# Performance work log

Hardware: AMD Instinct MI355X
Metric: run time of the kernel (lower is better)

## Reference

```python
import jax, jax.numpy as jnp
import numpy as np

N = 50000      # nodes
E = 400000     # edges
IN = 128       # in_channels
HID = 64       # hidden_channels (per head)
H = 4          # heads
OUT = 10       # classes
G = 64         # graphs in batch


def setup_inputs() -> dict:
    key = jax.random.key(0)
    ks = jax.random.split(key, 32)
    s = 0.05
    inp = {
        "x": jax.random.normal(ks[0], (N, IN), dtype=jnp.float32),
        "edge_index": jax.random.randint(ks[1], (2, E), 0, N, dtype=jnp.int32),
        "batch": jnp.sort(jax.random.randint(ks[2], (N,), 0, G, dtype=jnp.int32)),
    }
    # TransformerConv layer 1 params (in=IN -> heads*HID)
    d1 = H * HID
    inp["Wq1"] = jax.random.normal(ks[3], (IN, d1)) * s
    inp["bq1"] = jnp.zeros((d1,), jnp.float32)
    inp["Wk1"] = jax.random.normal(ks[4], (IN, d1)) * s
    inp["bk1"] = jnp.zeros((d1,), jnp.float32)
    inp["Wv1"] = jax.random.normal(ks[5], (IN, d1)) * s
    inp["bv1"] = jnp.zeros((d1,), jnp.float32)
    inp["Ws1"] = jax.random.normal(ks[6], (IN, d1)) * s   # root/skip weight
    inp["bs1"] = jnp.zeros((d1,), jnp.float32)
    # TransformerConv layer 2 params (in=H*HID -> heads*HID)
    inp["Wq2"] = jax.random.normal(ks[7], (d1, d1)) * s
    inp["bq2"] = jnp.zeros((d1,), jnp.float32)
    inp["Wk2"] = jax.random.normal(ks[8], (d1, d1)) * s
    inp["bk2"] = jnp.zeros((d1,), jnp.float32)
    inp["Wv2"] = jax.random.normal(ks[9], (d1, d1)) * s
    inp["bv2"] = jnp.zeros((d1,), jnp.float32)
    inp["Ws2"] = jax.random.normal(ks[10], (d1, d1)) * s
    inp["bs2"] = jnp.zeros((d1,), jnp.float32)
    # final classifier
    inp["Wl"] = jax.random.normal(ks[11], (d1, OUT)) * s
    inp["bl"] = jnp.zeros((OUT,), jnp.float32)
    return inp


def transformer_conv(x, src, dst, Wq, bq, Wk, bk, Wv, bv, Ws, bs):
    """PyG TransformerConv (concat=True, root_weight=True, beta=None, eval mode).
    src = edge_index[0] (source j), dst = edge_index[1] (target i).
    """
    n = x.shape[0]
    q = (x @ Wq + bq).reshape(n, H, HID)
    k = (x @ Wk + bk).reshape(n, H, HID)
    v = (x @ Wv + bv).reshape(n, H, HID)
    # per-edge attention logits [E, H]
    alpha = jnp.einsum('ehc,ehc->eh', q[dst], k[src]) / np.sqrt(HID).astype(np.float32)
    # scatter-softmax over incoming edges of each target node
    amax = jax.ops.segment_max(alpha, dst, num_segments=n)           # [N, H], -inf for isolated
    ex = jnp.exp(alpha - amax[dst])                                   # [E, H]
    denom = jax.ops.segment_sum(ex, dst, num_segments=n) + 1e-16      # [N, H]
    w = ex / denom[dst]                                               # normalized alpha [E, H]
    # scatter-sum aggregation of weighted values
    out = jax.ops.segment_sum(w[:, :, None] * v[src], dst, num_segments=n)  # [N, H, HID]
    out = out.reshape(n, H * HID)
    return out + (x @ Ws + bs)  # root/skip connection


def reference(x, edge_index, batch,
              Wq1, bq1, Wk1, bk1, Wv1, bv1, Ws1, bs1,
              Wq2, bq2, Wk2, bk2, Wv2, bv2, Ws2, bs2,
              Wl, bl):
    src, dst = edge_index[0], edge_index[1]
    h = jax.nn.elu(transformer_conv(x, src, dst, Wq1, bq1, Wk1, bk1, Wv1, bv1, Ws1, bs1))
    h = jax.nn.elu(transformer_conv(h, src, dst, Wq2, bq2, Wk2, bk2, Wv2, bv2, Ws2, bs2))
    # global mean pool per graph
    sums = jax.ops.segment_sum(h, batch, num_segments=G)              # [G, H*HID]
    cnt = jax.ops.segment_sum(jnp.ones((h.shape[0],), h.dtype), batch, num_segments=G)
    pooled = sums / jnp.maximum(cnt, 1.0)[:, None]
    logits = pooled @ Wl + bl
    return jax.nn.log_softmax(logits, axis=-1)
```

## Files before the change

kernel.cpp:

```cpp
#include <hip/hip_runtime.h>
#include <math.h>

constexpr int NN   = 50000;
constexpr int NE   = 400000;
constexpr int INC  = 128;
constexpr int NH   = 4;
constexpr int D1   = 256;
constexpr int D4   = 1024;
constexpr int NOUT = 10;
constexpr int NG   = 64;
constexpr int NB_SCAN = (NN + 255) / 256;


typedef __attribute__((ext_vector_type(8))) short bf16x8;
typedef __attribute__((ext_vector_type(4))) float f32x4;
typedef __attribute__((ext_vector_type(2))) float f32x2;

__device__ __forceinline__ short f2b(float f) {
  union { float f; unsigned int i; } v; v.f = f;
  unsigned int x = v.i;
  return (short)((x + 0x7FFFu + ((x >> 16) & 1u)) >> 16);
}
__device__ __forceinline__ float b2f(short u) {
  union { unsigned int i; float f; } v; v.i = ((unsigned int)(unsigned short)u) << 16;
  return v.f;
}
__device__ __forceinline__ float4 ld4b(const short* p) {
  short4 u = *(const short4*)p;
  return make_float4(b2f(u.x), b2f(u.y), b2f(u.z), b2f(u.w));
}
__device__ __forceinline__ int cvt_pk_bf16(float lo, float hi) {
  int r;
  asm volatile("v_cvt_pk_bf16_f32 %0, %1, %2" : "=v"(r) : "v"(lo), "v"(hi));
  return r;
}
__device__ __forceinline__ int pk_fp8x4(float a, float b, float c, float d) {
  int v = __builtin_amdgcn_cvt_pk_fp8_f32(a, b, 0, false);
  v = __builtin_amdgcn_cvt_pk_fp8_f32(c, d, v, true);
  return v;
}

__device__ __forceinline__ void gld_lds16(const short* g, short* l) {
  __builtin_amdgcn_global_load_lds(
      (const __attribute__((address_space(1))) unsigned int*)g,
      (__attribute__((address_space(3))) unsigned int*)l, 16, 0, 0);
}

constexpr int CVT_XB  = (NN * INC / 4 + 255) / 256;
constexpr int CVT_W1B = (4 * D1 * INC + 255) / 256;
constexpr int CVT_W2B = (4 * D1 * D1 + 255) / 256;
constexpr int CVT_BB  = 8;
constexpr int CVT_DB  = (NN + 255) / 256;
constexpr int CVT_SB  = (NG * D1 + 255) / 256;

__device__ __forceinline__ void wt_one(const float* Wq, const float* Wk,
    const float* Wv, const float* Ws, short* Wt, int kbits, int i) {
  int K = 1 << kbits;
  int seg = i >> (kbits + 8);
  int rem = i & ((D1 << kbits) - 1);
  int n = rem & (D1 - 1), k = rem >> 8;
  const float* W = (seg == 0) ? Wq : (seg == 1) ? Wk : (seg == 2) ? Wv : Ws;
  int row;
  if (seg == 0)      row = n;
  else if (seg == 3) row = 768 + n;
  else               row = 256 + (n >> 2) * 8 + ((seg == 2) ? 4 : 0) + (n & 3);
  Wt[(size_t)row * K + k] = f2b(W[(size_t)k * D1 + n]);
}

__global__ void cvt_all_k(const float* __restrict__ x, short* __restrict__ Xb,
    const float* __restrict__ Wq1, const float* __restrict__ Wk1,
    const float* __restrict__ Wv1, const float* __restrict__ Ws1,
    const float* __restrict__ Wq2, const float* __restrict__ Wk2,
    const float* __restrict__ Wv2, const float* __restrict__ Ws2,
    short* __restrict__ Wtc1, short* __restrict__ Wtc2,
    const float* __restrict__ bq1, const float* __restrict__ bk1,
    const float* __restrict__ bv1, const float* __restrict__ bs1,
    const float* __restrict__ bq2, const float* __restrict__ bk2,
    const float* __restrict__ bv2, const float* __restrict__ bs2,
    float* __restrict__ bc1, float* __restrict__ bc2,
    int* __restrict__ deg, float* __restrict__ sums) {
  const int b = blockIdx.x;
  const int t = threadIdx.x;
  if (b < CVT_XB) {
    int i = (b * 256 + t) * 4;
    if (i >= NN * INC) return;
    float4 v = *(const float4*)(x + i);
    short4 o; o.x = f2b(v.x); o.y = f2b(v.y); o.z = f2b(v.z); o.w = f2b(v.w);
    *(short4*)(Xb + i) = o;
  } else if (b < CVT_XB + CVT_W1B) {
    int i = (b - CVT_XB) * 256 + t;
    if (i < 4 * D1 * INC) wt_one(Wq1, Wk1, Wv1, Ws1, Wtc1, 7, i);
  } else if (b < CVT_XB + CVT_W1B + CVT_W2B) {
    int i = (b - CVT_XB - CVT_W1B) * 256 + t;
    if (i < 4 * D1 * D1) wt_one(Wq2, Wk2, Wv2, Ws2, Wtc2, 8, i);
  } else if (b < CVT_XB + CVT_W1B + CVT_W2B + CVT_BB) {
    int i = (b - CVT_XB - CVT_W1B - CVT_W2B) * 256 + t;
    if (i >= 2 * D4) return;
    int row = i & (D4 - 1);
    const float* bq = (i < D4) ? bq1 : bq2;
    const float* bk = (i < D4) ? bk1 : bk2;
    const float* bv = (i < D4) ? bv1 : bv2;
    const float* bs = (i < D4) ? bs1 : bs2;
    float v;
    if (row < 256) v = bq[row];
    else if (row < 768) {
      int j = row - 256, grp = j >> 3, off = j & 7;
      int ch = grp * 4 + (off & 3);
      v = (off < 4) ? bk[ch] : bv[ch];
    } else v = bs[row - 768];
    ((i < D4) ? bc1 : bc2)[row] = v;
  } else if (b < CVT_XB + CVT_W1B + CVT_W2B + CVT_BB + CVT_DB) {
    int i = (b - CVT_XB - CVT_W1B - CVT_W2B - CVT_BB) * 256 + t;
    if (i < NN) deg[i] = 0;
  } else {
    int i = (b - CVT_XB - CVT_W1B - CVT_W2B - CVT_BB - CVT_DB) * 256 + t;
    if (i < NG * D1) sums[i] = 0.f;
  }
}

__global__ void deg_count(const int* __restrict__ dst, int* __restrict__ deg) {
  int e = blockIdx.x * 256 + threadIdx.x;
  if (e < NE) atomicAdd(&deg[dst[e]], 1);
}
__global__ __launch_bounds__(256) void scan1(const int* __restrict__ deg,
    int* __restrict__ partial, const int* __restrict__ batch, int* __restrict__ gb) {
  if (blockIdx.x == NB_SCAN) {
    int g = threadIdx.x;
    if (g > NG) return;
    int lo = 0, hi = NN;
    while (lo < hi) {
      int mid = (lo + hi) >> 1;
      if (batch[mid] < g) lo = mid + 1; else hi = mid;
    }
    gb[g] = lo;
    return;
  }
  __shared__ int sh[256];
  int t = threadIdx.x, i = blockIdx.x * 256 + t;
  sh[t] = (i < NN) ? deg[i] : 0;
  __syncthreads();
  for (int off = 128; off > 0; off >>= 1) {
    if (t < off) sh[t] += sh[t + off];
    __syncthreads();
  }
  if (t == 0) partial[blockIdx.x] = sh[0];
}
__global__ __launch_bounds__(256) void scan3(const int* __restrict__ deg,
    const int* __restrict__ partial, int* __restrict__ rowstart,
    int* __restrict__ cursor) {
  __shared__ int sh[256];
  __shared__ int base_s;
  const int t = threadIdx.x;
  int pv = (t < NB_SCAN) ? partial[t] : 0;
  sh[t] = pv;
  __syncthreads();
  for (int off = 1; off < 256; off <<= 1) {
    int o = (t >= off) ? sh[t - off] : 0;
    __syncthreads();
    sh[t] += o;
    __syncthreads();
  }
  if (t == 0) base_s = (blockIdx.x == 0) ? 0 : sh[blockIdx.x - 1];
  __syncthreads();
  const int base = base_s;
  __syncthreads();
  int i = blockIdx.x * 256 + t;
  int v = (i < NN) ? deg[i] : 0;
  sh[t] = v;
  __syncthreads();
  for (int off = 1; off < 256; off <<= 1) {
    int o = (t >= off) ? sh[t - off] : 0;
    __syncthreads();
    sh[t] += o;
    __syncthreads();
  }
  int excl = sh[t] - v + base;
  if (i <= NN) rowstart[i] = excl;
  if (i < NN)  cursor[i]   = excl;
}
__global__ void scatter_k(const int* __restrict__ src, const int* __restrict__ dst,
    int* __restrict__ cursor, int* __restrict__ esrc) {
  int e = blockIdx.x * 256 + threadIdx.x;
  if (e >= NE) return;
  int d = dst[e];
  int pos = atomicAdd(&cursor[d], 1);
  esrc[pos] = src[e];
}

constexpr int CLDS = 136;

__global__ __launch_bounds__(256, 4) void gemm_mfma(
    const short* __restrict__ Xb, const short* __restrict__ Wt,
    const float* __restrict__ bias, short* __restrict__ QS,
    unsigned char* __restrict__ KV8, int M, int K) {
  __shared__ short smem[16384];
  const int bx = blockIdx.x;
  const int by = blockIdx.y;
  const int m_tile = (bx & 7) + (by << 3);
  const int n_tile = bx >> 3;
  const int m0 = m_tile * 128;
  if (m0 >= M) return;
  const int n0 = n_tile * 128;

  const int t    = threadIdx.x;
  const int lane = t & 63;
  const int wv   = t >> 6;
  const int wm   = (wv >> 1) * 64;
  const int wn   = (wv & 1) * 64;
  const int quad = lane >> 4;
  const int l16  = lane & 15;
  const int lrow = lane >> 2;
  const int lseg = lane & 3;

  const int swz_w = (lseg ^ ((lrow >> 1) & 3)) * 8;
  const int swz_r = (quad ^ ((l16 >> 1) & 3)) * 8;

  f32x4 acc[4][4] = {};

  {
#pragma unroll
    for (int j = 0; j < 2; ++j) {
      const int rb = (wv * 2 + j) * 16;
      int gm = m0 + rb + lrow;
      gm = gm < M ? gm : M - 1;
      gld_lds16(Xb + (size_t)gm * K + swz_w,              &smem[rb * 32]);
      gld_lds16(Wt + (size_t)(n0 + rb + lrow) * K + swz_w, &smem[4096 + rb * 32]);
    }
  }
  __syncthreads();

  int cur = 0;
  for (int k0 = 0; k0 < K; k0 += 32) {
    if (k0 + 32 < K) {
      short* An = &smem[(cur ^ 1) * 8192];
      short* Bn = &smem[(cur ^ 1) * 8192 + 4096];
#pragma unroll
      for (int j = 0; j < 2; ++j) {
        const int rb = (wv * 2 + j) * 16;
        int gm = m0 + rb + lrow;
        gm = gm < M ? gm : M - 1;
        gld_lds16(Xb + (size_t)gm * K + k0 + 32 + swz_w,              &An[rb * 32]);
        gld_lds16(Wt + (size_t)(n0 + rb + lrow) * K + k0 + 32 + swz_w, &Bn[rb * 32]);
      }
    }
    {
      const short* Ac = &smem[cur * 8192];
      const short* Bc = &smem[cur * 8192 + 4096];
      bf16x8 a[4], b[4];
#pragma unroll
      for (int mi = 0; mi < 4; mi++)
        a[mi] = *(const bf16x8*)(&Ac[(wm + mi * 16 + l16) * 32 + swz_r]);
#pragma unroll
      for (int nj = 0; nj < 4; nj++)
        b[nj] = *(const bf16x8*)(&Bc[(wn + nj * 16 + l16) * 32 + swz_r]);
#pragma unroll
      for (int mi = 0; mi < 4; mi++)
#pragma unroll
        for (int nj = 0; nj < 4; nj++)
          acc[mi][nj] = __builtin_amdgcn_mfma_f32_16x16x32_bf16(b[nj], a[mi], acc[mi][nj], 0, 0, 0);
    }
    __syncthreads();
    cur ^= 1;
  }

  const bool isKV = (n_tile >= 2) && (n_tile <= 5);
  float4 bz[4];
#pragma unroll
  for (int nj = 0; nj < 4; nj++)
    bz[nj] = *(const float4*)(bias + n0 + wn + nj * 16 + quad * 4);
  const int kv_base = n0 - 256;
  const int qs_base = (n_tile < 2) ? n0 : (n0 - 512);

#pragma unroll
  for (int p = 0; p < 2; ++p) {
    if ((wv >> 1) == p) {
      if (isKV) {
        unsigned char* cs = (unsigned char*)smem;
#pragma unroll
        for (int mi = 0; mi < 4; mi++) {
          const int row = mi * 16 + l16;
#pragma unroll
          for (int nj = 0; nj < 4; nj++) {
            const int colb = wn + nj * 16 + quad * 4;
            const int pk = pk_fp8x4(acc[mi][nj][0] + bz[nj].x, acc[mi][nj][1] + bz[nj].y,
                                    acc[mi][nj][2] + bz[nj].z, acc[mi][nj][3] + bz[nj].w);
            *(int*)(cs + row * 136 + colb) = pk;
          }
        }
      } else {
#pragma unroll
        for (int mi = 0; mi < 4; mi++) {
          const int row = mi * 16 + l16;
#pragma unroll
          for (int nj = 0; nj < 4; nj++) {
            const int col = wn + nj * 16 + quad * 4;
            int2 o;
            o.x = cvt_pk_bf16(acc[mi][nj][0] + bz[nj].x, acc[mi][nj][1] + bz[nj].y);
            o.y = cvt_pk_bf16(acc[mi][nj][2] + bz[nj].z, acc[mi][nj][3] + bz[nj].w);
            *(int2*)(&smem[row * CLDS + col]) = o;
          }
        }
      }
    }
    __syncthreads();
    if (isKV) {
      const unsigned char* cs = (const unsigned char*)smem;
#pragma unroll
      for (int it = 0; it < 4; ++it) {
        const int chunk = it * 256 + t;
        const int row = chunk >> 4;
        const int cb  = (chunk & 15) * 8;
        const int gm  = m0 + p * 64 + row;
        if (gm < M)
          *(int2*)(KV8 + (size_t)gm * 512 + kv_base + cb) = *(const int2*)(cs + row * 136 + cb);
      }
    } else {
#pragma unroll
      for (int it = 0; it < 4; ++it) {
        const int chunk = it * 256 + t;
        const int row = chunk >> 4;
        const int cc  = (chunk & 15) * 8;
        const int gm  = m0 + p * 64 + row;
        if (gm < M)
          *(int4*)(QS + (size_t)gm * 512 + qs_base + cc) = *(const int4*)(&smem[row * CLDS + cc]);
      }
    }
    if (p == 0) __syncthreads();
  }
}

__device__ __forceinline__ f32x2 cvt_lo(int x) { return __builtin_amdgcn_cvt_pk_f32_fp8(x, false); }
__device__ __forceinline__ f32x2 cvt_hi(int x) { return __builtin_amdgcn_cvt_pk_f32_fp8(x, true); }

template <int CTRL>
__device__ __forceinline__ float ror_add(float x) {
  int y = __builtin_amdgcn_update_dpp(0, __float_as_int(x), CTRL, 0xF, 0xF, true);
  return x + __int_as_float(y);
}
__device__ __forceinline__ float red16(float x) {
  x = ror_add<0x121>(x);
  x = ror_add<0x122>(x);
  x = ror_add<0x124>(x);
  x = ror_add<0x128>(x);
  return x;
}

#define SC2 (0.125f * 1.44269504088896341f)

__device__ __forceinline__ float edge_score(const int2 x, f32x2 q01, f32x2 q23,
                                            f32x2& vv01, f32x2& vv23) {
  f32x2 kk01 = cvt_lo(x.x), kk23 = cvt_hi(x.x);
  vv01 = cvt_lo(x.y); vv23 = cvt_hi(x.y);
  f32x2 dd = q01 * kk01;
  dd += q23 * kk23;
  return red16(dd.x + dd.y);
}

template <typename TOUT>
__device__ __forceinline__ void st1(TOUT* p, float v);
template <> __device__ __forceinline__ void st1<float>(float* p, float v) { *p = v; }
template <> __device__ __forceinline__ void st1<short>(short* p, float v) { *p = f2b(v); }

template <typename TOUT>
__global__ __launch_bounds__(256) void node_attn(
    const int* __restrict__ rowstart, const int* __restrict__ esrc,
    const short* __restrict__ QS, const unsigned char* __restrict__ KV8,
    TOUT* __restrict__ out) {
  const int nid = blockIdx.x * 4 + (threadIdx.x >> 6);
  if (nid >= NN) return;
  const int t  = threadIdx.x & 63;
  const int c0 = t * 4;
  const int r0 = __builtin_amdgcn_readfirstlane(rowstart[nid]);
  const int r1 = __builtin_amdgcn_readfirstlane(rowstart[nid + 1]);
  const short4 qu = *(const short4*)(QS + (size_t)nid * 512 + c0);
  const f32x2 q01 = {b2f(qu.x) * SC2, b2f(qu.y) * SC2};
  const f32x2 q23 = {b2f(qu.z) * SC2, b2f(qu.w) * SC2};
  const unsigned char* kvb = KV8 + t * 8;
  float m = -INFINITY, denom = 0.f;
  f32x2 a01 = {0.f, 0.f}, a23 = {0.f, 0.f};
  int r = r0;
  for (; r + 7 < r1; r += 8) {
    const int e0 = __builtin_amdgcn_readfirstlane(esrc[r + 0]);
    const int e1 = __builtin_amdgcn_readfirstlane(esrc[r + 1]);
    const int e2 = __builtin_amdgcn_readfirstlane(esrc[r + 2]);
    const int e3 = __builtin_amdgcn_readfirstlane(esrc[r + 3]);
    const int e4 = __builtin_amdgcn_readfirstlane(esrc[r + 4]);
    const int e5 = __builtin_amdgcn_readfirstlane(esrc[r + 5]);
    const int e6 = __builtin_amdgcn_readfirstlane(esrc[r + 6]);
    const int e7 = __builtin_amdgcn_readfirstlane(esrc[r + 7]);
    const int2 x0 = *(const int2*)(kvb + (size_t)e0 * 512);
    const int2 x1 = *(const int2*)(kvb + (size_t)e1 * 512);
    const int2 x2 = *(const int2*)(kvb + (size_t)e2 * 512);
    const int2 x3 = *(const int2*)(kvb + (size_t)e3 * 512);
    const int2 x4 = *(const int2*)(kvb + (size_t)e4 * 512);
    const int2 x5 = *(const int2*)(kvb + (size_t)e5 * 512);
    const int2 x6 = *(const int2*)(kvb + (size_t)e6 * 512);
    const int2 x7 = *(const int2*)(kvb + (size_t)e7 * 512);
    f32x2 v01_0, v23_0, v01_1, v23_1, v01_2, v23_2, v01_3, v23_3;
    f32x2 v01_4, v23_4, v01_5, v23_5, v01_6, v23_6, v01_7, v23_7;
    const float s0 = edge_score(x0, q01, q23, v01_0, v23_0);
    const float s1 = edge_score(x1, q01, q23, v01_1, v23_1);
    const float s2 = edge_score(x2, q01, q23, v01_2, v23_2);
    const float s3 = edge_score(x3, q01, q23, v01_3, v23_3);
    const float s4 = edge_score(x4, q01, q23, v01_4, v23_4);
    const float s5 = edge_score(x5, q01, q23, v01_5, v23_5);
    const float s6 = edge_score(x6, q01, q23, v01_6, v23_6);
    const float s7 = edge_score(x7, q01, q23, v01_7, v23_7);
    const float t01 = fmaxf(s0, s1), t23 = fmaxf(s2, s3);
    const float t45 = fmaxf(s4, s5), t67 = fmaxf(s6, s7);
    const float nm = fmaxf(fmaxf(m, fmaxf(t01, t23)), fmaxf(t45, t67));
    const float sc  = exp2f(m - nm);
    const float ex0 = exp2f(s0 - nm);
    const float ex1 = exp2f(s1 - nm);
    const float ex2 = exp2f(s2 - nm);
    const float ex3 = exp2f(s3 - nm);
    const float ex4 = exp2f(s4 - nm);
    const float ex5 = exp2f(s5 - nm);
    const float ex6 = exp2f(s6 - nm);
    const float ex7 = exp2f(s7 - nm);
    denom = denom * sc + ((ex0 + ex1) + (ex2 + ex3)) + ((ex4 + ex5) + (ex6 + ex7));
    const f32x2 scv = {sc, sc};
    a01 = a01 * scv; a23 = a23 * scv;
    a01 += f32x2{ex0, ex0} * v01_0; a23 += f32x2{ex0, ex0} * v23_0;
    a01 += f32x2{ex1, ex1} * v01_1; a23 += f32x2{ex1, ex1} * v23_1;
    a01 += f32x2{ex2, ex2} * v01_2; a23 += f32x2{ex2, ex2} * v23_2;
    a01 += f32x2{ex3, ex3} * v01_3; a23 += f32x2{ex3, ex3} * v23_3;
    a01 += f32x2{ex4, ex4} * v01_4; a23 += f32x2{ex4, ex4} * v23_4;
    a01 += f32x2{ex5, ex5} * v01_5; a23 += f32x2{ex5, ex5} * v23_5;
    a01 += f32x2{ex6, ex6} * v01_6; a23 += f32x2{ex6, ex6} * v23_6;
    a01 += f32x2{ex7, ex7} * v01_7; a23 += f32x2{ex7, ex7} * v23_7;
    m = nm;
  }
  for (; r + 3 < r1; r += 4) {
    const int e0 = __builtin_amdgcn_readfirstlane(esrc[r + 0]);
    const int e1 = __builtin_amdgcn_readfirstlane(esrc[r + 1]);
    const int e2 = __builtin_amdgcn_readfirstlane(esrc[r + 2]);
    const int e3 = __builtin_amdgcn_readfirstlane(esrc[r + 3]);
    const int2 x0 = *(const int2*)(kvb + (size_t)e0 * 512);
    const int2 x1 = *(const int2*)(kvb + (size_t)e1 * 512);
    const int2 x2 = *(const int2*)(kvb + (size_t)e2 * 512);
    const int2 x3 = *(const int2*)(kvb + (size_t)e3 * 512);
    f32x2 v01_0, v23_0, v01_1, v23_1, v01_2, v23_2, v01_3, v23_3;
    const float s0 = edge_score(x0, q01, q23, v01_0, v23_0);
    const float s1 = edge_score(x1, q01, q23, v01_1, v23_1);
    const float s2 = edge_score(x2, q01, q23, v01_2, v23_2);
    const float s3 = edge_score(x3, q01, q23, v01_3, v23_3);
    const float nm = fmaxf(fmaxf(m, fmaxf(s0, s1)), fmaxf(s2, s3));
    const float sc  = exp2f(m - nm);
    const float ex0 = exp2f(s0 - nm);
    const float ex1 = exp2f(s1 - nm);
    const float ex2 = exp2f(s2 - nm);
    const float ex3 = exp2f(s3 - nm);
    denom = denom * sc + ex0 + ex1 + ex2 + ex3;
    const f32x2 scv = {sc, sc};
    a01 = a01 * scv; a23 = a23 * scv;
    a01 += f32x2{ex0, ex0} * v01_0; a23 += f32x2{ex0, ex0} * v23_0;
    a01 += f32x2{ex1, ex1} * v01_1; a23 += f32x2{ex1, ex1} * v23_1;
    a01 += f32x2{ex2, ex2} * v01_2; a23 += f32x2{ex2, ex2} * v23_2;
    a01 += f32x2{ex3, ex3} * v01_3; a23 += f32x2{ex3, ex3} * v23_3;
    m = nm;
  }
  for (; r < r1; r++) {
    const int e0 = __builtin_amdgcn_readfirstlane(esrc[r]);
    const int2 x0 = *(const int2*)(kvb + (size_t)e0 * 512);
    f32x2 v01_0, v23_0;
    const float s0 = edge_score(x0, q01, q23, v01_0, v23_0);
    const float nm = fmaxf(m, s0);
    const float sc  = exp2f(m - nm);
    const float ex0 = exp2f(s0 - nm);
    denom = denom * sc + ex0;
    const f32x2 scv = {sc, sc};
    a01 = a01 * scv; a23 = a23 * scv;
    a01 += f32x2{ex0, ex0} * v01_0; a23 += f32x2{ex0, ex0} * v23_0;
    m = nm;
  }
  const float inv = 1.0f / (denom + 1e-16f);
  const float4 sk = ld4b(QS + (size_t)nid * 512 + 256 + c0);
  float o0 = a01.x * inv + sk.x;
  float o1 = a01.y * inv + sk.y;
  float o2 = a23.x * inv + sk.z;
  float o3 = a23.y * inv + sk.w;
  o0 = o0 > 0.f ? o0 : expm1f(o0);
  o1 = o1 > 0.f ? o1 : expm1f(o1);
  o2 = o2 > 0.f ? o2 : expm1f(o2);
  o3 = o3 > 0.f ? o3 : expm1f(o3);
  TOUT* p = out + (size_t)nid * D1 + c0;
  st1<TOUT>(p + 0, o0); st1<TOUT>(p + 1, o1);
  st1<TOUT>(p + 2, o2); st1<TOUT>(p + 3, o3);
}

__global__ __launch_bounds__(256) void pool_k(const short* __restrict__ h,
    const int* __restrict__ batch, const int* __restrict__ gb,
    float* __restrict__ sums) {
  const int c = threadIdx.x;
  const int n0 = blockIdx.x * 64;
  const int n1 = min(n0 + 64, NN);
  const int g0 = batch[n0];
  const int g1 = batch[n1 - 1];
  for (int g = g0; g <= g1; ++g) {
    const int a = max(gb[g], n0);
    const int b = min(gb[g + 1], n1);
    if (b <= a) continue;
    float s0 = 0.f, s1 = 0.f, s2 = 0.f, s3 = 0.f;
    int n = a;
    for (; n + 3 < b; n += 4) {
      s0 += b2f(h[(size_t)(n + 0) * D1 + c]);
      s1 += b2f(h[(size_t)(n + 1) * D1 + c]);
      s2 += b2f(h[(size_t)(n + 2) * D1 + c]);
      s3 += b2f(h[(size_t)(n + 3) * D1 + c]);
    }
    for (; n < b; ++n) s0 += b2f(h[(size_t)n * D1 + c]);
    atomicAdd(&sums[(size_t)g * D1 + c], (s0 + s1) + (s2 + s3));
  }
}

__global__ __launch_bounds__(640) void head_k(const float* __restrict__ sums,
    const int* __restrict__ gb, const float* __restrict__ Wl,
    const float* __restrict__ bl, float* __restrict__ out) {
  __shared__ float logits[NG][NOUT];
  const int t = threadIdx.x;
  if (t < NG * NOUT) {
    int g = t / NOUT, o = t % NOUT;
    float inv = 1.0f / fmaxf((float)(gb[g + 1] - gb[g]), 1.0f);
    float acc = 0.f;
    for (int k = 0; k < D1; k++) acc += sums[(size_t)g * D1 + k] * Wl[k * NOUT + o];
    logits[g][o] = acc * inv + bl[o];
  }
  __syncthreads();
  if (t < NG) {
    float mx = -INFINITY;
#pragma unroll
    for (int o = 0; o < NOUT; o++) mx = fmaxf(mx, logits[t][o]);
    float s = 0.f;
#pragma unroll
    for (int o = 0; o < NOUT; o++) s += __expf(logits[t][o] - mx);
    float lse = mx + logf(s);
#pragma unroll
    for (int o = 0; o < NOUT; o++) out[t * NOUT + o] = logits[t][o] - lse;
  }
}

extern "C" void kernel_launch(void* const* d_in, const int* in_sizes, int n_in,
                              void* d_out, int out_size, void* d_ws, size_t ws_size,
                              hipStream_t stream) {
  const float* x   = (const float*)d_in[0];
  const int* ei    = (const int*)d_in[1];
  const int* batch = (const int*)d_in[2];
  const float* Wq1 = (const float*)d_in[3];  const float* bq1 = (const float*)d_in[4];
  const float* Wk1 = (const float*)d_in[5];  const float* bk1 = (const float*)d_in[6];
  const float* Wv1 = (const float*)d_in[7];  const float* bv1 = (const float*)d_in[8];
  const float* Ws1 = (const float*)d_in[9];  const float* bs1 = (const float*)d_in[10];
  const float* Wq2 = (const float*)d_in[11]; const float* bq2 = (const float*)d_in[12];
  const float* Wk2 = (const float*)d_in[13]; const float* bk2 = (const float*)d_in[14];
  const float* Wv2 = (const float*)d_in[15]; const float* bv2 = (const float*)d_in[16];
  const float* Ws2 = (const float*)d_in[17]; const float* bs2 = (const float*)d_in[18];
  const float* Wl  = (const float*)d_in[19]; const float* bl  = (const float*)d_in[20];

  const int* srcIdx = ei;
  const int* dstIdx = ei + NE;

  float* ws = (float*)d_ws;
  const size_t SZ_NODE = (size_t)NN * D1;
  float* H2f  = ws;
  short* H2b  = (short*)H2f;
  float* sums = ws + SZ_NODE;
  float* bc1  = sums + (size_t)NG * D1;
  float* bc2  = bc1 + D4;
  short* Xb   = (short*)(bc2 + D4);
  short* H1b  = Xb + (size_t)NN * INC;
  short* QS   = H1b + SZ_NODE;
  short* Wtc1 = QS + (size_t)NN * 512;
  short* Wtc2 = Wtc1 + (size_t)D4 * INC;
  unsigned char* KV8 = (unsigned char*)(Wtc2 + (size_t)D4 * D1);
  int* ip      = (int*)(KV8 + (size_t)NN * 512);
  int* deg     = ip;
  int* partial = deg + NN;
  int* rowstart= partial + 256;
  int* cursor  = rowstart + NN + 1;
  int* esrc    = cursor + NN;
  int* gb      = esrc + NE;

  const int mtiles = (NN + 127) / 128;
  const dim3 gemmGrid(64, (mtiles + 7) / 8);
  const int edgeBlocks = (NE + 255) / 256;
  const int aggBlocks  = (NN + 3) / 4;
  const int cvtBlocks  = CVT_XB + CVT_W1B + CVT_W2B + CVT_BB + CVT_DB + CVT_SB;

  cvt_all_k<<<cvtBlocks, 256, 0, stream>>>(x, Xb,
      Wq1, Wk1, Wv1, Ws1, Wq2, Wk2, Wv2, Ws2, Wtc1, Wtc2,
      bq1, bk1, bv1, bs1, bq2, bk2, bv2, bs2, bc1, bc2, deg, sums);

  deg_count<<<edgeBlocks, 256, 0, stream>>>(dstIdx, deg);
  scan1<<<NB_SCAN + 1, 256, 0, stream>>>(deg, partial, batch, gb);
  scan3<<<NB_SCAN, 256, 0, stream>>>(deg, partial, rowstart, cursor);
  scatter_k<<<edgeBlocks, 256, 0, stream>>>(srcIdx, dstIdx, cursor, esrc);

  gemm_mfma<<<gemmGrid, 256, 0, stream>>>(Xb, Wtc1, bc1, QS, KV8, NN, INC);
  node_attn<short><<<aggBlocks, 256, 0, stream>>>(rowstart, esrc, QS, KV8, H1b);

  gemm_mfma<<<gemmGrid, 256, 0, stream>>>(H1b, Wtc2, bc2, QS, KV8, NN, D1);
  node_attn<short><<<aggBlocks, 256, 0, stream>>>(rowstart, esrc, QS, KV8, H2b);

  pool_k<<<(NN + 63) / 64, 256, 0, stream>>>(H2b, batch, gb, sums);
  head_k<<<1, 640, 0, stream>>>(sums, gb, Wl, bl, (float*)d_out);
}
```

Measured before the change: 341.5 us.

## Fuse scan into single-pass decoupled lookback, merge pool and head, vectorize weight conversion

Replaces the two-kernel degree scan with one kernel that uses a decoupled-lookback prefix scan with atomic descriptors. It also fuses global mean pooling and the classifier head into a single kernel with one block per graph, which removes the sums buffer and its atomics. Weight transposition now writes 8 bf16 values per thread as one 16-byte store. Together these cut launch count and atomic traffic. In exchange, the lookback spin depends on forward progress across blocks, and the pool kernel has only 64 blocks for the full node reduction.

```diff
diff --git a/kernel.cpp b/kernel.cpp
--- a/kernel.cpp
+++ b/kernel.cpp
@@ -47,24 +47,31 @@
 }
 
 constexpr int CVT_XB  = (NN * INC / 4 + 255) / 256;
-constexpr int CVT_W1B = (4 * D1 * INC + 255) / 256;
-constexpr int CVT_W2B = (4 * D1 * D1 + 255) / 256;
+constexpr int CVT_W1B = (4 * D1 * INC / 8 + 255) / 256;
+constexpr int CVT_W2B = (4 * D1 * D1 / 8 + 255) / 256;
 constexpr int CVT_BB  = 8;
 constexpr int CVT_DB  = (NN + 255) / 256;
-constexpr int CVT_SB  = (NG * D1 + 255) / 256;
-
-__device__ __forceinline__ void wt_one(const float* Wq, const float* Wk,
+constexpr int CVT_FB  = 1;
+
+__device__ __forceinline__ void wt_one8(const float* Wq, const float* Wk,
     const float* Wv, const float* Ws, short* Wt, int kbits, int i) {
-  int K = 1 << kbits;
-  int seg = i >> (kbits + 8);
-  int rem = i & ((D1 << kbits) - 1);
-  int n = rem & (D1 - 1), k = rem >> 8;
+  const int K = 1 << kbits;
+  const int row = i >> (kbits - 3);
+  const int k0 = (i & ((K >> 3) - 1)) << 3;
+  int seg, n;
+  if (row < 256)      { seg = 0; n = row; }
+  else if (row < 768) { int j = row - 256, off = j & 7;
+                        seg = (off >= 4) ? 2 : 1; n = (j >> 3) * 4 + (off & 3); }
+  else                { seg = 3; n = row - 768; }
   const float* W = (seg == 0) ? Wq : (seg == 1) ? Wk : (seg == 2) ? Wv : Ws;
-  int row;
-  if (seg == 0)      row = n;
-  else if (seg == 3) row = 768 + n;
-  else               row = 256 + (n >> 2) * 8 + ((seg == 2) ? 4 : 0) + (n & 3);
-  Wt[(size_t)row * K + k] = f2b(W[(size_t)k * D1 + n]);
+  short o[8];
+#pragma unroll
+  for (int kk = 0; kk < 8; kk++) o[kk] = f2b(W[(size_t)(k0 + kk) * D1 + n]);
+  int4 pk;
+  short* ps = (short*)&pk;
+#pragma unroll
+  for (int kk = 0; kk < 8; kk++) ps[kk] = o[kk];
+  *(int4*)(Wt + (size_t)row * K + k0) = pk;
 }
 
 __global__ void cvt_all_k(const float* __restrict__ x, short* __restrict__ Xb,
@@ -78,7 +85,7 @@
     const float* __restrict__ bq2, const float* __restrict__ bk2,
     const float* __restrict__ bv2, const float* __restrict__ bs2,
     float* __restrict__ bc1, float* __restrict__ bc2,
-    int* __restrict__ deg, float* __restrict__ sums) {
+    int* __restrict__ deg, unsigned int* __restrict__ desc) {
   const int b = blockIdx.x;
   const int t = threadIdx.x;
   if (b < CVT_XB) {
@@ -89,10 +96,10 @@
     *(short4*)(Xb + i) = o;
   } else if (b < CVT_XB + CVT_W1B) {
     int i = (b - CVT_XB) * 256 + t;
-    if (i < 4 * D1 * INC) wt_one(Wq1, Wk1, Wv1, Ws1, Wtc1, 7, i);
+    if (i < 4 * D1 * INC / 8) wt_one8(Wq1, Wk1, Wv1, Ws1, Wtc1, 7, i);
   } else if (b < CVT_XB + CVT_W1B + CVT_W2B) {
     int i = (b - CVT_XB - CVT_W1B) * 256 + t;
-    if (i < 4 * D1 * D1) wt_one(Wq2, Wk2, Wv2, Ws2, Wtc2, 8, i);
+    if (i < 4 * D1 * D1 / 8) wt_one8(Wq2, Wk2, Wv2, Ws2, Wtc2, 8, i);
   } else if (b < CVT_XB + CVT_W1B + CVT_W2B + CVT_BB) {
     int i = (b - CVT_XB - CVT_W1B - CVT_W2B) * 256 + t;
     if (i >= 2 * D4) return;
@@ -113,8 +120,7 @@
     int i = (b - CVT_XB - CVT_W1B - CVT_W2B - CVT_BB) * 256 + t;
     if (i < NN) deg[i] = 0;
   } else {
-    int i = (b - CVT_XB - CVT_W1B - CVT_W2B - CVT_BB - CVT_DB) * 256 + t;
-    if (i < NG * D1) sums[i] = 0.f;
+    if (t < NB_SCAN) desc[t] = 0u;
   }
 }
 
@@ -122,50 +128,26 @@
   int e = blockIdx.x * 256 + threadIdx.x;
   if (e < NE) atomicAdd(&deg[dst[e]], 1);
 }
-__global__ __launch_bounds__(256) void scan1(const int* __restrict__ deg,
-    int* __restrict__ partial, const int* __restrict__ batch, int* __restrict__ gb) {
-  if (blockIdx.x == NB_SCAN) {
-    int g = threadIdx.x;
-    if (g > NG) return;
+
+__global__ __launch_bounds__(256) void scan_k(const int* __restrict__ deg,
+    const int* __restrict__ batch, unsigned int* __restrict__ desc,
+    int* __restrict__ rowstart, int* __restrict__ cursor, int* __restrict__ gb) {
+  const int b = blockIdx.x;
+  const int t = threadIdx.x;
+  if (b == NB_SCAN) {
+    if (t > NG) return;
     int lo = 0, hi = NN;
     while (lo < hi) {
       int mid = (lo + hi) >> 1;
-      if (batch[mid] < g) lo = mid + 1; else hi = mid;
-    }
-    gb[g] = lo;
+      if (batch[mid] < t) lo = mid + 1; else hi = mid;
+    }
+    gb[t] = lo;
     return;
   }
-  __shared__ int sh[256];
-  int t = threadIdx.x, i = blockIdx.x * 256 + t;
-  sh[t] = (i < NN) ? deg[i] : 0;
-  __syncthreads();
-  for (int off = 128; off > 0; off >>= 1) {
-    if (t < off) sh[t] += sh[t + off];
-    __syncthreads();
-  }
-  if (t == 0) partial[blockIdx.x] = sh[0];
-}
-__global__ __launch_bounds__(256) void scan3(const int* __restrict__ deg,
-    const int* __restrict__ partial, int* __restrict__ rowstart,
-    int* __restrict__ cursor) {
   __shared__ int sh[256];
   __shared__ int base_s;
-  const int t = threadIdx.x;
-  int pv = (t < NB_SCAN) ? partial[t] : 0;
-  sh[t] = pv;
-  __syncthreads();
-  for (int off = 1; off < 256; off <<= 1) {
-    int o = (t >= off) ? sh[t - off] : 0;
-    __syncthreads();
-    sh[t] += o;
-    __syncthreads();
-  }
-  if (t == 0) base_s = (blockIdx.x == 0) ? 0 : sh[blockIdx.x - 1];
-  __syncthreads();
-  const int base = base_s;
-  __syncthreads();
-  int i = blockIdx.x * 256 + t;
-  int v = (i < NN) ? deg[i] : 0;
+  const int i = b * 256 + t;
+  const int v = (i < NN) ? deg[i] : 0;
   sh[t] = v;
   __syncthreads();
   for (int off = 1; off < 256; off <<= 1) {
@@ -174,10 +156,37 @@
     sh[t] += o;
     __syncthreads();
   }
-  int excl = sh[t] - v + base;
+  const int incl = sh[t];
+  const int aggr = sh[255];
+  if (t == 0) {
+    if (b == 0) {
+      __hip_atomic_store(&desc[0], ((unsigned int)aggr << 2) | 2u,
+                         __ATOMIC_RELEASE, __HIP_MEMORY_SCOPE_AGENT);
+      base_s = 0;
+    } else {
+      __hip_atomic_store(&desc[b], ((unsigned int)aggr << 2) | 1u,
+                         __ATOMIC_RELEASE, __HIP_MEMORY_SCOPE_AGENT);
+      int base = 0;
+      int j = b - 1;
+      while (j >= 0) {
+        unsigned int d = __hip_atomic_load(&desc[j], __ATOMIC_ACQUIRE,
+                                           __HIP_MEMORY_SCOPE_AGENT);
+        unsigned int st = d & 3u;
+        if (st == 2u)      { base += (int)(d >> 2); break; }
+        else if (st == 1u) { base += (int)(d >> 2); j--; }
+        else               { __builtin_amdgcn_s_sleep(2); }
+      }
+      __hip_atomic_store(&desc[b], ((unsigned int)(base + aggr) << 2) | 2u,
+                         __ATOMIC_RELEASE, __HIP_MEMORY_SCOPE_AGENT);
+      base_s = base;
+    }
+  }
+  __syncthreads();
+  const int excl = base_s + incl - v;
   if (i <= NN) rowstart[i] = excl;
   if (i < NN)  cursor[i]   = excl;
 }
+
 __global__ void scatter_k(const int* __restrict__ src, const int* __restrict__ dst,
     int* __restrict__ cursor, int* __restrict__ esrc) {
   int e = blockIdx.x * 256 + threadIdx.x;
@@ -489,54 +498,48 @@
   st1<TOUT>(p + 2, o2); st1<TOUT>(p + 3, o3);
 }
 
-__global__ __launch_bounds__(256) void pool_k(const short* __restrict__ h,
-    const int* __restrict__ batch, const int* __restrict__ gb,
-    float* __restrict__ sums) {
-  const int c = threadIdx.x;
-  const int n0 = blockIdx.x * 64;
-  const int n1 = min(n0 + 64, NN);
-  const int g0 = batch[n0];
-  const int g1 = batch[n1 - 1];
-  for (int g = g0; g <= g1; ++g) {
-    const int a = max(gb[g], n0);
-    const int b = min(gb[g + 1], n1);
-    if (b <= a) continue;
-    float s0 = 0.f, s1 = 0.f, s2 = 0.f, s3 = 0.f;
-    int n = a;
-    for (; n + 3 < b; n += 4) {
-      s0 += b2f(h[(size_t)(n + 0) * D1 + c]);
-      s1 += b2f(h[(size_t)(n + 1) * D1 + c]);
-      s2 += b2f(h[(size_t)(n + 2) * D1 + c]);
-      s3 += b2f(h[(size_t)(n + 3) * D1 + c]);
-    }
-    for (; n < b; ++n) s0 += b2f(h[(size_t)n * D1 + c]);
-    atomicAdd(&sums[(size_t)g * D1 + c], (s0 + s1) + (s2 + s3));
-  }
-}
-
-__global__ __launch_bounds__(640) void head_k(const float* __restrict__ sums,
+__global__ __launch_bounds__(1024) void pool_head_k(const short* __restrict__ h,
     const int* __restrict__ gb, const float* __restrict__ Wl,
     const float* __restrict__ bl, float* __restrict__ out) {
-  __shared__ float logits[NG][NOUT];
+  __shared__ float sh4[1024];
+  __shared__ float mlds[D1];
+  __shared__ float lgs[NOUT];
+  const int g = blockIdx.x;
   const int t = threadIdx.x;
-  if (t < NG * NOUT) {
-    int g = t / NOUT, o = t % NOUT;
-    float inv = 1.0f / fmaxf((float)(gb[g + 1] - gb[g]), 1.0f);
-    float acc = 0.f;
-    for (int k = 0; k < D1; k++) acc += sums[(size_t)g * D1 + k] * Wl[k * NOUT + o];
-    logits[g][o] = acc * inv + bl[o];
-  }
+  const int c = t & (D1 - 1);
+  const int no = t >> 8;
+  const int a = gb[g], b = gb[g + 1];
+  float s = 0.f;
+  for (int n = a + no; n < b; n += 4) s += b2f(h[(size_t)n * D1 + c]);
+  sh4[t] = s;
   __syncthreads();
-  if (t < NG) {
-    float mx = -INFINITY;
-#pragma unroll
-    for (int o = 0; o < NOUT; o++) mx = fmaxf(mx, logits[t][o]);
-    float s = 0.f;
-#pragma unroll
-    for (int o = 0; o < NOUT; o++) s += __expf(logits[t][o] - mx);
-    float lse = mx + logf(s);
-#pragma unroll
-    for (int o = 0; o < NOUT; o++) out[t * NOUT + o] = logits[t][o] - lse;
+  if (no == 0) {
+    const float inv = 1.0f / fmaxf((float)(b - a), 1.0f);
+    mlds[c] = (sh4[c] + sh4[c + 256] + sh4[c + 512] + sh4[c + 768]) * inv;
+  }
+  __syncthreads();
+  if (t < 64) {
+#pragma unroll
+    for (int o = 0; o < NOUT; o++) {
+      float p = 0.f;
+#pragma unroll
+      for (int q = 0; q < 4; q++)
+        p += mlds[t + q * 64] * Wl[(t + q * 64) * NOUT + o];
+#pragma unroll
+      for (int off = 1; off < 64; off <<= 1) p += __shfl_xor(p, off, 64);
+      if (t == 0) lgs[o] = p + bl[o];
+    }
+    if (t == 0) {
+      float mx = -INFINITY;
+#pragma unroll
+      for (int o = 0; o < NOUT; o++) mx = fmaxf(mx, lgs[o]);
+      float se = 0.f;
+#pragma unroll
+      for (int o = 0; o < NOUT; o++) se += __expf(lgs[o] - mx);
+      const float lse = mx + logf(se);
+#pragma unroll
+      for (int o = 0; o < NOUT; o++) out[g * NOUT + o] = lgs[o] - lse;
+    }
   }
 }
 
@@ -561,10 +564,8 @@
 
   float* ws = (float*)d_ws;
   const size_t SZ_NODE = (size_t)NN * D1;
-  float* H2f  = ws;
-  short* H2b  = (short*)H2f;
-  float* sums = ws + SZ_NODE;
-  float* bc1  = sums + (size_t)NG * D1;
+  short* H2b  = (short*)ws;
+  float* bc1  = ws + SZ_NODE;
   float* bc2  = bc1 + D4;
   short* Xb   = (short*)(bc2 + D4);
   short* H1b  = Xb + (size_t)NN * INC;
@@ -574,8 +575,8 @@
   unsigned char* KV8 = (unsigned char*)(Wtc2 + (size_t)D4 * D1);
   int* ip      = (int*)(KV8 + (size_t)NN * 512);
   int* deg     = ip;
-  int* partial = deg + NN;
-  int* rowstart= partial + 256;
+  unsigned int* desc = (unsigned int*)(deg + NN);
+  int* rowstart= (int*)(desc + 256);
   int* cursor  = rowstart + NN + 1;
   int* esrc    = cursor + NN;
   int* gb      = esrc + NE;
@@ -584,15 +585,14 @@
   const dim3 gemmGrid(64, (mtiles + 7) / 8);
   const int edgeBlocks = (NE + 255) / 256;
   const int aggBlocks  = (NN + 3) / 4;
-  const int cvtBlocks  = CVT_XB + CVT_W1B + CVT_W2B + CVT_BB + CVT_DB + CVT_SB;
+  const int cvtBlocks  = CVT_XB + CVT_W1B + CVT_W2B + CVT_BB + CVT_DB + CVT_FB;
 
   cvt_all_k<<<cvtBlocks, 256, 0, stream>>>(x, Xb,
       Wq1, Wk1, Wv1, Ws1, Wq2, Wk2, Wv2, Ws2, Wtc1, Wtc2,
-      bq1, bk1, bv1, bs1, bq2, bk2, bv2, bs2, bc1, bc2, deg, sums);
+      bq1, bk1, bv1, bs1, bq2, bk2, bv2, bs2, bc1, bc2, deg, desc);
 
   deg_count<<<edgeBlocks, 256, 0, stream>>>(dstIdx, deg);
-  scan1<<<NB_SCAN + 1, 256, 0, stream>>>(deg, partial, batch, gb);
-  scan3<<<NB_SCAN, 256, 0, stream>>>(deg, partial, rowstart, cursor);
+  scan_k<<<NB_SCAN + 1, 256, 0, stream>>>(deg, batch, desc, rowstart, cursor, gb);
   scatter_k<<<edgeBlocks, 256, 0, stream>>>(srcIdx, dstIdx, cursor, esrc);
 
   gemm_mfma<<<gemmGrid, 256, 0, stream>>>(Xb, Wtc1, bc1, QS, KV8, NN, INC);
@@ -601,6 +601,5 @@
   gemm_mfma<<<gemmGrid, 256, 0, stream>>>(H1b, Wtc2, bc2, QS, KV8, NN, D1);
   node_attn<short><<<aggBlocks, 256, 0, stream>>>(rowstart, esrc, QS, KV8, H2b);
 
-  pool_k<<<(NN + 63) / 64, 256, 0, stream>>>(H2b, batch, gb, sums);
-  head_k<<<1, 640, 0, stream>>>(sums, gb, Wl, bl, (float*)d_out);
-}
+  pool_head_k<<<NG, 1024, 0, stream>>>(H2b, gb, Wl, bl, (float*)d_out);
+}
```

Result: slower. 397.8 us (+16.5%).
